# Optimization experiments

Measured on AMD Instinct MI355X. Metric: run time of the kernel, lower is better.

## Reference

```python
import jax, jax.numpy as jnp
import numpy as np

R = 2            # connect_gap -> disk radius for morphological closing
N_ITER = 24      # fixed thinning iteration count (jit-compatible stand-in for run-to-convergence)

_yy, _xx = np.mgrid[-R:R + 1, -R:R + 1]
DISK = ((_xx ** 2 + _yy ** 2) <= R * R).astype(np.float32)  # skimage.morphology.disk(2): 5x5, 13 ones
DISK_SUM = float(DISK.sum())


def _conv2d(x, k):
    # x: [D,H,W] float32, k: [kh,kw]; per-slice SAME conv (D acts as batch)
    return jax.lax.conv_general_dilated(x[:, None], k[None, None], (1, 1), 'SAME')[:, 0]


def _closing(mask):
    # binary closing = erosion(dilation(mask)) with disk footprint (zero padding at borders)
    k = jnp.asarray(DISK)
    dil = _conv2d(mask.astype(jnp.float32), k) > 0.5
    ero = _conv2d(dil.astype(jnp.float32), k) > (DISK_SUM - 0.5)
    return ero


def _neighbors(img):
    # 8-neighborhood P2..P9 (N, NE, E, SE, S, SW, W, NW), zero-padded borders
    p = jnp.pad(img, ((0, 0), (1, 1), (1, 1)))
    return (p[:, :-2, 1:-1], p[:, :-2, 2:], p[:, 1:-1, 2:], p[:, 2:, 2:],
            p[:, 2:, 1:-1], p[:, 2:, :-2], p[:, 1:-1, :-2], p[:, :-2, :-2])


def _subiter(img, step):
    # one Zhang-Suen thinning sub-iteration over all slices/voxels at once
    P = _neighbors(img)
    Pi = [q.astype(jnp.int32) for q in P]
    B = sum(Pi)                                   # number of ON neighbors
    seq = Pi + [Pi[0]]
    A = sum(((seq[k] == 0) & (seq[k + 1] == 1)).astype(jnp.int32) for k in range(8))
    cB = (B >= 2) & (B <= 6)
    cA = A == 1
    if step == 0:
        c3 = ~(P[0] & P[2] & P[4])   # P2*P4*P6 == 0
        c4 = ~(P[2] & P[4] & P[6])   # P4*P6*P8 == 0
    else:
        c3 = ~(P[0] & P[2] & P[6])   # P2*P4*P8 == 0
        c4 = ~(P[0] & P[4] & P[6])   # P2*P6*P8 == 0
    return img & ~(img & cB & cA & c3 & c4)


def _skeletonize(mask):
    def body(img, _):
        img = _subiter(img, 0)
        img = _subiter(img, 1)
        return img, None
    out, _ = jax.lax.scan(body, mask, None, length=N_ITER)
    return out


def setup_inputs() -> dict:
    key = jax.random.key(0)
    gt_skel = jax.random.uniform(key, (1, 64, 512, 512), dtype=jnp.float32)
    return {"gt_skel": gt_skel}


def reference(gt_skel):
    mask = gt_skel[0] > 0.5          # squeeze leading dim; binary foreground mask [D,H,W]
    skel = _skeletonize(_closing(mask))
    return skel[None]                # [1,D,H,W] bool
```

## Files before the change

### kernel.cpp

```cpp
#include <hip/hip_runtime.h>
#include <stdint.h>

#define DD    64
#define HH    512
#define WWID  512
#define WPR   8
#define NSUB  48
#define BANDS 4
#define BH    128
#define HALO  52
#define MAXR  (BH + 2*HALO)
#define ARR   (MAXR + 4)
#define PITCH 10

typedef unsigned long long u64;

__global__ void pack_kernel(const float* __restrict__ in, u64* __restrict__ bits) {
    long gid  = (long)blockIdx.x * blockDim.x + threadIdx.x;
    long wv   = gid >> 6;
    int  lane = (int)(gid & 63);
    long base = wv * 256;
    #pragma unroll
    for (int k = 0; k < 4; ++k) {
        float v = in[base + (long)k * 64 + lane];
        u64 m = __ballot(v > 0.5f);
        if (lane == 0) bits[wv * 4 + k] = m;
    }
}

__device__ __forceinline__ void fadd(u64 a, u64 b, u64 c, u64& s, u64& co) {
    u64 t = a ^ b;
    s  = t ^ c;
    co = (a & b) | (t & c);
}
__device__ __forceinline__ void hadd(u64 a, u64 b, u64& s, u64& co) {
    s = a ^ b; co = a & b;
}

__global__ __launch_bounds__(512, 1)
void thin_kernel(const u64* __restrict__ bits, int* __restrict__ out) {
    __shared__ u64 bufA[ARR][PITCH];
    __shared__ u64 bufB[ARR][PITCH];

    const int blk  = blockIdx.x;
    const int z    = blk >> 2;
    const int band = blk & 3;
    const int r0   = band * BH;
    const int la   = (r0 - HALO > 0) ? (r0 - HALO) : 0;
    const int lb   = (r0 + BH + HALO < HH) ? (r0 + BH + HALO) : HH;
    const int nrows = lb - la;
    const int ob0  = r0 - la;

    const int t  = threadIdx.x;
    const int lr = t >> 1;
    const int h4 = (t & 1) * 4;
    const int ar = lr + 2;

    {
        u64* fa = &bufA[0][0];
        u64* fb = &bufB[0][0];
        for (int i = t; i < ARR * PITCH; i += 512) { fa[i] = 0; fb[i] = 0; }
    }
    __syncthreads();

    if (lr < nrows) {
        const u64* src = bits + ((long)(z * HH + la + lr)) * WPR + h4;
        ulonglong2 v0 = *reinterpret_cast<const ulonglong2*>(src);
        ulonglong2 v1 = *reinterpret_cast<const ulonglong2*>(src + 2);
        bufA[ar][h4 + 1] = v0.x;
        bufA[ar][h4 + 2] = v0.y;
        bufA[ar][h4 + 3] = v1.x;
        bufA[ar][h4 + 4] = v1.y;
    }
    __syncthreads();

    u64 (*cur)[PITCH] = bufA;
    u64 (*nxt)[PITCH] = bufB;

    #pragma unroll 1
    for (int phase = 0; phase < 2; ++phase) {
        if (lr < nrows) {
            u64 w[5][6];
            #pragma unroll
            for (int rr = 0; rr < 5; ++rr) {
                #pragma unroll
                for (int q = 0; q < 3; ++q) {
                    ulonglong2 v = *reinterpret_cast<const ulonglong2*>(&cur[ar - 2 + rr][h4 + 2 * q]);
                    w[rr][2 * q]     = v.x;
                    w[rr][2 * q + 1] = v.y;
                }
            }
            u64 res[4];
            #pragma unroll
            for (int jj = 0; jj < 4; ++jj) {
                u64 c  = w[2][jj + 1], pl = w[2][jj], pr = w[2][jj + 2];
                u64 l1 = (c << 1) | (pl >> 63);
                u64 l2 = (c << 2) | (pl >> 62);
                u64 r1 = (c >> 1) | (pr << 63);
                u64 r2 = (c >> 2) | (pr << 62);
                u64 u  = w[1][jj + 1];
                u64 ul = (u << 1) | (w[1][jj] >> 63);
                u64 ur = (u >> 1) | (w[1][jj + 2] << 63);
                u64 d  = w[3][jj + 1];
                u64 dl = (d << 1) | (w[3][jj] >> 63);
                u64 dr = (d >> 1) | (w[3][jj + 2] << 63);
                u64 u2 = w[0][jj + 1];
                u64 d2 = w[4][jj + 1];
                res[jj] = (phase == 0)
                    ? (c | l1 | l2 | r1 | r2 | u | ul | ur | d | dl | dr | u2 | d2)
                    : (c & l1 & l2 & r1 & r2 & u & ul & ur & d & dl & dr & u2 & d2);
            }
            #pragma unroll
            for (int jj = 0; jj < 4; ++jj) nxt[ar][h4 + 1 + jj] = res[jj];
        }
        __syncthreads();
        u64 (*tmp)[PITCH] = cur; cur = nxt; nxt = tmp;
    }

    #pragma unroll 1
    for (int it = 0; it < NSUB / 2; ++it) {
        #pragma unroll
        for (int sub = 0; sub < 2; ++sub) {
            const int k  = 2 * it + sub + 1;
            const int hw = NSUB - k;
            int lo = ob0 - hw;       if (lo < 0) lo = 0;
            int hi = ob0 + BH + hw;  if (hi > nrows) hi = nrows;
            if (lr >= lo && lr < hi) {
                u64 w[3][6];
                #pragma unroll
                for (int rr = 0; rr < 3; ++rr) {
                    #pragma unroll
                    for (int q = 0; q < 3; ++q) {
                        ulonglong2 v = *reinterpret_cast<const ulonglong2*>(&cur[ar - 1 + rr][h4 + 2 * q]);
                        w[rr][2 * q]     = v.x;
                        w[rr][2 * q + 1] = v.y;
                    }
                }
                u64 res[4];
                #pragma unroll
                for (int jj = 0; jj < 4; ++jj) {
                    u64 c  = w[1][jj + 1];
                    u64 N  = w[0][jj + 1];
                    u64 S  = w[2][jj + 1];
                    u64 E  = (w[1][jj + 1] >> 1) | (w[1][jj + 2] << 63);
                    u64 Wn = (w[1][jj + 1] << 1) | (w[1][jj]     >> 63);
                    u64 NE = (w[0][jj + 1] >> 1) | (w[0][jj + 2] << 63);
                    u64 NW = (w[0][jj + 1] << 1) | (w[0][jj]     >> 63);
                    u64 SE = (w[2][jj + 1] >> 1) | (w[2][jj + 2] << 63);
                    u64 SW = (w[2][jj + 1] << 1) | (w[2][jj]    >> 63);
                    u64 p[8] = {N, NE, E, SE, S, SW, Wn, NW};
                    u64 one = 0, two = 0;
                    #pragma unroll
                    for (int q = 0; q < 8; ++q) {
                        u64 tk = ~p[q] & p[(q + 1) & 7];
                        two |= one & tk;
                        one |= tk;
                    }
                    u64 A1 = one & ~two;
                    u64 sa, ca, sb, cb2, sc, cc;
                    fadd(p[0], p[1], p[2], sa, ca);
                    fadd(p[3], p[4], p[5], sb, cb2);
                    hadd(p[6], p[7], sc, cc);
                    u64 S0, cd; fadd(sa, sb, sc, S0, cd);
                    u64 t2, ce; fadd(ca, cb2, cc, t2, ce);
                    u64 S1, cf; hadd(cd, t2, S1, cf);
                    u64 S2, S3; hadd(ce, cf, S2, S3);
                    u64 Bge2 = S1 | S2 | S3;
                    u64 Ble6 = ~((S2 & S1 & S0) | S3);
                    u64 cB   = Bge2 & Ble6;
                    u64 c3, c4;
                    if (sub == 0) { c3 = ~(N & E & S);  c4 = ~(E & S & Wn); }
                    else          { c3 = ~(N & E & Wn); c4 = ~(N & S & Wn); }
                    res[jj] = c & ~(cB & A1 & c3 & c4);
                }
                #pragma unroll
                for (int jj = 0; jj < 4; ++jj) nxt[ar][h4 + 1 + jj] = res[jj];
            }
            __syncthreads();
            u64 (*tmp)[PITCH] = cur; cur = nxt; nxt = tmp;
        }
    }

    const long slice_base = (long)z * HH * WWID;
    for (int e = t; e < BH * (WWID / 4); e += 512) {
        int rr  = e >> 7;
        int x4  = e & 127;
        int gr  = r0 + rr;
        int arr = (gr - la) + 2;
        int col = x4 * 4;
        u64 w  = cur[arr][1 + (col >> 6)];
        int sh = col & 63;
        int4 f;
        f.x = (int)((w >> (sh + 0)) & 1ull);
        f.y = (int)((w >> (sh + 1)) & 1ull);
        f.z = (int)((w >> (sh + 2)) & 1ull);
        f.w = (int)((w >> (sh + 3)) & 1ull);
        *reinterpret_cast<int4*>(out + slice_base + (long)gr * WWID + col) = f;
    }
}

extern "C" void kernel_launch(void* const* d_in, const int* in_sizes, int n_in,
                              void* d_out, int out_size, void* d_ws, size_t ws_size,
                              hipStream_t stream) {
    const float* in   = (const float*)d_in[0];
    int*         out  = (int*)d_out;
    u64*         bits = (u64*)d_ws;

    pack_kernel<<<16384, 256, 0, stream>>>(in, bits);
    thin_kernel<<<DD * BANDS, 512, 0, stream>>>(bits, out);
}
```

Measured before the change: 135.1 us.

## Add early exit on thinning convergence and skip uniform-neighborhood waves

Adds a per-block flag set whenever any pixel changes in an iteration and leaves the thinning loop once a full iteration changes nothing. Also detects wavefronts whose 3x3 neighborhoods are all-on or all-off and copies the center unchanged, skipping the Zhang-Suen logic. The sub loop is no longer unrolled, and extra ballots and shared flag writes are added to each sub-iteration. For random inputs the early exit may rarely trigger, and the halo-shrinking schedule still assumes a fixed count.

Result: slower. 163.7 us (+21.2%).

```diff
diff --git a/kernel.cpp b/kernel.cpp
--- a/kernel.cpp
+++ b/kernel.cpp
@@ -5,7 +5,7 @@
 #define HH    512
 #define WWID  512
 #define WPR   8
-#define NSUB  48
+#define NITER 24
 #define BANDS 4
 #define BH    128
 #define HALO  52
@@ -41,6 +41,7 @@
 void thin_kernel(const u64* __restrict__ bits, int* __restrict__ out) {
     __shared__ u64 bufA[ARR][PITCH];
     __shared__ u64 bufB[ARR][PITCH];
+    __shared__ unsigned int flags[2];
 
     const int blk  = blockIdx.x;
     const int z    = blk >> 2;
@@ -60,6 +61,7 @@
         u64* fa = &bufA[0][0];
         u64* fb = &bufB[0][0];
         for (int i = t; i < ARR * PITCH; i += 512) { fa[i] = 0; fb[i] = 0; }
+        if (t < 2) flags[t] = 0u;
     }
     __syncthreads();
 
@@ -118,13 +120,15 @@
     }
 
     #pragma unroll 1
-    for (int it = 0; it < NSUB / 2; ++it) {
-        #pragma unroll
+    for (int it2 = 0; it2 < NITER; ++it2) {
+        #pragma unroll 1
         for (int sub = 0; sub < 2; ++sub) {
-            const int k  = 2 * it + sub + 1;
-            const int hw = NSUB - k;
+            const int k  = 2 * it2 + sub + 1;
+            const int hw = 2 * NITER - k;
             int lo = ob0 - hw;       if (lo < 0) lo = 0;
             int hi = ob0 + BH + hw;  if (hi > nrows) hi = nrows;
+
+            u64 changed = 0;
             if (lr >= lo && lr < hi) {
                 u64 w[3][6];
                 #pragma unroll
@@ -136,49 +140,67 @@
                         w[rr][2 * q + 1] = v.y;
                     }
                 }
+                u64 cc[4], Nv[4], Sv[4], Ev[4], Wv[4], NEv[4], NWv[4], SEv[4], SWv[4];
+                u64 mixedany = 0;
+                #pragma unroll
+                for (int jj = 0; jj < 4; ++jj) {
+                    cc[jj] = w[1][jj + 1];
+                    Nv[jj] = w[0][jj + 1];
+                    Sv[jj] = w[2][jj + 1];
+                    Ev[jj]  = (w[1][jj + 1] >> 1) | (w[1][jj + 2] << 63);
+                    Wv[jj]  = (w[1][jj + 1] << 1) | (w[1][jj]     >> 63);
+                    NEv[jj] = (w[0][jj + 1] >> 1) | (w[0][jj + 2] << 63);
+                    NWv[jj] = (w[0][jj + 1] << 1) | (w[0][jj]     >> 63);
+                    SEv[jj] = (w[2][jj + 1] >> 1) | (w[2][jj + 2] << 63);
+                    SWv[jj] = (w[2][jj + 1] << 1) | (w[2][jj]     >> 63);
+                    u64 sol = cc[jj] & Nv[jj] & Sv[jj] & Ev[jj] & Wv[jj] & NEv[jj] & NWv[jj] & SEv[jj] & SWv[jj];
+                    u64 anv = cc[jj] | Nv[jj] | Sv[jj] | Ev[jj] | Wv[jj] | NEv[jj] | NWv[jj] | SEv[jj] | SWv[jj];
+                    mixedany |= anv ^ sol;
+                }
                 u64 res[4];
-                #pragma unroll
-                for (int jj = 0; jj < 4; ++jj) {
-                    u64 c  = w[1][jj + 1];
-                    u64 N  = w[0][jj + 1];
-                    u64 S  = w[2][jj + 1];
-                    u64 E  = (w[1][jj + 1] >> 1) | (w[1][jj + 2] << 63);
-                    u64 Wn = (w[1][jj + 1] << 1) | (w[1][jj]     >> 63);
-                    u64 NE = (w[0][jj + 1] >> 1) | (w[0][jj + 2] << 63);
-                    u64 NW = (w[0][jj + 1] << 1) | (w[0][jj]     >> 63);
-                    u64 SE = (w[2][jj + 1] >> 1) | (w[2][jj + 2] << 63);
-                    u64 SW = (w[2][jj + 1] << 1) | (w[2][jj]    >> 63);
-                    u64 p[8] = {N, NE, E, SE, S, SW, Wn, NW};
-                    u64 one = 0, two = 0;
+                if (__ballot(mixedany != 0) == 0) {
                     #pragma unroll
-                    for (int q = 0; q < 8; ++q) {
-                        u64 tk = ~p[q] & p[(q + 1) & 7];
-                        two |= one & tk;
-                        one |= tk;
+                    for (int jj = 0; jj < 4; ++jj) res[jj] = cc[jj];
+                } else {
+                    #pragma unroll
+                    for (int jj = 0; jj < 4; ++jj) {
+                        u64 p[8] = {Nv[jj], NEv[jj], Ev[jj], SEv[jj], Sv[jj], SWv[jj], Wv[jj], NWv[jj]};
+                        u64 one = 0, two = 0;
+                        #pragma unroll
+                        for (int q = 0; q < 8; ++q) {
+                            u64 tk = ~p[q] & p[(q + 1) & 7];
+                            two |= one & tk;
+                            one |= tk;
+                        }
+                        u64 A1 = one & ~two;
+                        u64 sa, ca, sb, cb2, sc, cc2;
+                        fadd(p[0], p[1], p[2], sa, ca);
+                        fadd(p[3], p[4], p[5], sb, cb2);
+                        hadd(p[6], p[7], sc, cc2);
+                        u64 S0, cd; fadd(sa, sb, sc, S0, cd);
+                        u64 t2, ce; fadd(ca, cb2, cc2, t2, ce);
+                        u64 S1, cf; hadd(cd, t2, S1, cf);
+                        u64 S2, S3; hadd(ce, cf, S2, S3);
+                        u64 Bge2 = S1 | S2 | S3;
+                        u64 Ble6 = ~((S2 & S1 & S0) | S3);
+                        u64 cB   = Bge2 & Ble6;
+                        u64 c3, c4;
+                        if (sub == 0) { c3 = ~(Nv[jj] & Ev[jj] & Sv[jj]); c4 = ~(Ev[jj] & Sv[jj] & Wv[jj]); }
+                        else          { c3 = ~(Nv[jj] & Ev[jj] & Wv[jj]); c4 = ~(Nv[jj] & Sv[jj] & Wv[jj]); }
+                        res[jj] = cc[jj] & ~(cB & A1 & c3 & c4);
+                        changed |= res[jj] ^ cc[jj];
                     }
-                    u64 A1 = one & ~two;
-                    u64 sa, ca, sb, cb2, sc, cc;
-                    fadd(p[0], p[1], p[2], sa, ca);
-                    fadd(p[3], p[4], p[5], sb, cb2);
-                    hadd(p[6], p[7], sc, cc);
-                    u64 S0, cd; fadd(sa, sb, sc, S0, cd);
-                    u64 t2, ce; fadd(ca, cb2, cc, t2, ce);
-                    u64 S1, cf; hadd(cd, t2, S1, cf);
-                    u64 S2, S3; hadd(ce, cf, S2, S3);
-                    u64 Bge2 = S1 | S2 | S3;
-                    u64 Ble6 = ~((S2 & S1 & S0) | S3);
-                    u64 cB   = Bge2 & Ble6;
-                    u64 c3, c4;
-                    if (sub == 0) { c3 = ~(N & E & S);  c4 = ~(E & S & Wn); }
-                    else          { c3 = ~(N & E & Wn); c4 = ~(N & S & Wn); }
-                    res[jj] = c & ~(cB & A1 & c3 & c4);
                 }
                 #pragma unroll
                 for (int jj = 0; jj < 4; ++jj) nxt[ar][h4 + 1 + jj] = res[jj];
             }
+            u64 chb = __ballot(changed != 0);
+            if ((t & 63) == 0 && chb != 0) flags[it2 & 1] = 1u;
+            if (sub == 1 && t == 0) flags[(it2 + 1) & 1] = 0u;
             __syncthreads();
             u64 (*tmp)[PITCH] = cur; cur = nxt; nxt = tmp;
         }
+        if (flags[it2 & 1] == 0u) break;
     }
 
     const long slice_base = (long)z * HH * WWID;
```
